# Kernel optimization log

Measured on AMD Instinct MI355X. Metric: run time of the kernel, lower is better.

The kernel has to match this reference:

```python
import jax, jax.numpy as jnp
import numpy as np
import math

HIDDEN = 256
GUMBEL_EPS = 1e-20
MASK_EPS = 1e-8
TAU = 1.0


def _gumbel(u):
    return -jnp.log(-jnp.log(u + GUMBEL_EPS) + GUMBEL_EPS)


def setup_inputs() -> dict:
    key = jax.random.key(0)
    ks = jax.random.split(key, 16)
    B, N = 16, 128
    goal_dim, obs_dim, local_dim, num_skills = 64, 128, 64, 16
    h = HIDDEN

    def lin(k, out_d, in_d):
        kw, kb = jax.random.split(k)
        bound = 1.0 / math.sqrt(in_d)
        W = jax.random.uniform(kw, (out_d, in_d), minval=-bound, maxval=bound, dtype=jnp.float32)
        b = jax.random.uniform(kb, (out_d,), minval=-bound, maxval=bound, dtype=jnp.float32)
        return W, b

    Wq, bq = lin(ks[0], h, goal_dim)
    Wk, bk = lin(ks[1], h, obs_dim)
    Wv, bv = lin(ks[2], h, obs_dim)
    Wo, bo = lin(ks[3], h, h)
    Ws, bs = lin(ks[4], num_skills, local_dim + goal_dim + h)

    return {
        "goals": jax.random.normal(ks[5], (B, N, goal_dim), dtype=jnp.float32),
        "agents": jax.random.normal(ks[6], (B, N, obs_dim), dtype=jnp.float32),
        "agents_local": jax.random.normal(ks[7], (B, N, local_dim), dtype=jnp.float32),
        "u1": jax.random.uniform(ks[8], (B, N, N), dtype=jnp.float32),
        "u2": jax.random.uniform(ks[9], (B, N, N), dtype=jnp.float32),
        "Wq": Wq, "bq": bq, "Wk": Wk, "bk": bk, "Wv": Wv, "bv": bv,
        "Wo": Wo, "bo": bo, "Ws": Ws, "bs": bs,
    }


def reference(goals, agents, agents_local, u1, u2, Wq, bq, Wk, bk, Wv, bv, Wo, bo, Ws, bs):
    # Projections
    Q = jnp.einsum('bnd,hd->bnh', goals, Wq) + bq   # [B,N,h]
    K = jnp.einsum('bmd,hd->bmh', agents, Wk) + bk  # [B,N,h]
    V = jnp.einsum('bmd,hd->bmh', agents, Wv) + bv  # [B,N,h]

    scale = math.sqrt(HIDDEN) + 1e-12
    logits = jnp.einsum('bnh,bmh->bnm', Q, K) / scale  # [B,N,N]

    # Gumbel-sigmoid mask (soft, hard=False)
    g1, g2 = _gumbel(u1), _gumbel(u2)
    mask = jax.nn.sigmoid((logits + g1 - g2) / TAU)  # [B,N,N]

    scores = logits + jnp.log(mask + MASK_EPS)
    attn = jax.nn.softmax(scores, axis=-1)  # [B,N,N]

    # info[b,n,h] = sum_m attn[b,n,m] * mask[b,n,m] * V[b,m,h]
    # (equivalent to (attn.unsqueeze(-1) * V_masked).sum(dim=2) without
    #  materializing the [B,N,N,h] V_masked tensor)
    info = jnp.einsum('bnm,bnm,bmh->bnh', attn, mask, V)

    out = jnp.einsum('bnh,gh->bng', info, Wo) + bo  # [B,N,h]

    concat = jnp.concatenate([agents_local, goals, out], axis=-1)
    logit = jnp.einsum('bnc,sc->bns', concat, Ws) + bs  # [B,N,num_skills]

    return (logit, mask, attn, out)
```

## Files before the change

kernel.cpp:

```cpp
#include <hip/hip_runtime.h>
#include <math.h>


typedef float f32x4 __attribute__((ext_vector_type(4)));
typedef short s16x8 __attribute__((ext_vector_type(8)));

#define WOBF_OFF  0
#define QBF_OFF   32768
#define KBF_OFF   294912
#define VTBF_OFF  557056

#define LOGIT_OFF 0
#define MASK_OFF  32768
#define ATTN_OFF  294912
#define OUT_OFF   557056

static __device__ __forceinline__ unsigned short f2bf(float x) {
  unsigned int u = __float_as_uint(x);
  u = (u + 0x7fffu + ((u >> 16) & 1u)) >> 16;
  return (unsigned short)u;
}
static __device__ __forceinline__ float bf2f(unsigned short h) {
  return __uint_as_float(((unsigned int)h) << 16);
}

static __device__ __forceinline__ void split8(const float* __restrict__ p,
                                              s16x8* hi, s16x8* lo) {
  float4 x0 = *(const float4*)p;
  float4 x1 = *(const float4*)(p + 4);
  float xs[8] = {x0.x, x0.y, x0.z, x0.w, x1.x, x1.y, x1.z, x1.w};
#pragma unroll
  for (int j = 0; j < 8; j++) {
    unsigned short h = f2bf(xs[j]);
    (*hi)[j] = (short)h;
    (*lo)[j] = (short)f2bf(xs[j] - bf2f(h));
  }
}

__global__ __launch_bounds__(512) void proj_k(
    const float* __restrict__ goals, const float* __restrict__ agents,
    const float* __restrict__ Wq, const float* __restrict__ bq,
    const float* __restrict__ Wk, const float* __restrict__ bk,
    const float* __restrict__ Wv, const float* __restrict__ bv,
    const float* __restrict__ Wo, float* __restrict__ ws) {
  unsigned short* qbf  = (unsigned short*)(ws + QBF_OFF);
  unsigned short* kbf  = (unsigned short*)(ws + KBF_OFF);
  unsigned short* vtbf = (unsigned short*)(ws + VTBF_OFF);
  unsigned short* wobf = (unsigned short*)(ws + WOBF_OFF);

  __shared__ __align__(16) float xg[16 * 68];
  __shared__ __align__(16) float xa[16 * 132];

  int t = threadIdx.x;
  int bid = blockIdx.x;
  int xcd = bid & 7, j = bid >> 3;
  int bb = 2 * xcd + (j & 1);
  int sub = j >> 1;
  int r0 = bb * 128 + (sub >> 1) * 16;
  int colbase = (sub & 1) * 128;

  for (int i = t; i < 1024; i += 512) xg[(i >> 6) * 68 + (i & 63)] = goals[(size_t)r0 * 64 + i];
  for (int i = t; i < 2048; i += 512) xa[(i >> 7) * 132 + (i & 127)] = agents[(size_t)r0 * 128 + i];
  if (t < 256) {
    int jj = bid * 256 + t;
    wobf[jj] = f2bf(Wo[jj]);
  }
  __syncthreads();

  int w = t >> 6, l = t & 63, lr = l & 15, lc = l >> 4;
  int oc = colbase + w * 16 + lr;

  {
    f32x4 acc = {0.f, 0.f, 0.f, 0.f};
#pragma unroll
    for (int kk = 0; kk < 2; kk++) {
      s16x8 ahi, alo, bhi, blo;
      split8(&xg[lr * 68 + kk * 32 + lc * 8], &ahi, &alo);
      split8(&Wq[(size_t)oc * 64 + kk * 32 + lc * 8], &bhi, &blo);
      acc = __builtin_amdgcn_mfma_f32_16x16x32_bf16(ahi, bhi, acc, 0, 0, 0);
      acc = __builtin_amdgcn_mfma_f32_16x16x32_bf16(alo, bhi, acc, 0, 0, 0);
      acc = __builtin_amdgcn_mfma_f32_16x16x32_bf16(ahi, blo, acc, 0, 0, 0);
    }
    float bqv = bq[oc];
#pragma unroll
    for (int q = 0; q < 4; q++)
      qbf[(size_t)(r0 + 4 * lc + q) * 256 + oc] = f2bf(acc[q] + bqv);
  }
  {
    f32x4 acc = {0.f, 0.f, 0.f, 0.f};
#pragma unroll
    for (int kk = 0; kk < 4; kk++) {
      s16x8 ahi, alo, bhi, blo;
      split8(&xa[lr * 132 + kk * 32 + lc * 8], &ahi, &alo);
      split8(&Wk[(size_t)oc * 128 + kk * 32 + lc * 8], &bhi, &blo);
      acc = __builtin_amdgcn_mfma_f32_16x16x32_bf16(ahi, bhi, acc, 0, 0, 0);
      acc = __builtin_amdgcn_mfma_f32_16x16x32_bf16(alo, bhi, acc, 0, 0, 0);
      acc = __builtin_amdgcn_mfma_f32_16x16x32_bf16(ahi, blo, acc, 0, 0, 0);
    }
    float bkv = bk[oc];
#pragma unroll
    for (int q = 0; q < 4; q++)
      kbf[(size_t)(r0 + 4 * lc + q) * 256 + oc] = f2bf(acc[q] + bkv);
  }
  {
    f32x4 acc = {0.f, 0.f, 0.f, 0.f};
#pragma unroll
    for (int kk = 0; kk < 4; kk++) {
      s16x8 ahi, alo, bhi, blo;
      split8(&xa[lr * 132 + kk * 32 + lc * 8], &ahi, &alo);
      split8(&Wv[(size_t)oc * 128 + kk * 32 + lc * 8], &bhi, &blo);
      acc = __builtin_amdgcn_mfma_f32_16x16x32_bf16(ahi, bhi, acc, 0, 0, 0);
      acc = __builtin_amdgcn_mfma_f32_16x16x32_bf16(alo, bhi, acc, 0, 0, 0);
      acc = __builtin_amdgcn_mfma_f32_16x16x32_bf16(ahi, blo, acc, 0, 0, 0);
    }
    float bvv = bv[oc];
    int m0 = r0 & 127;
#pragma unroll
    for (int q = 0; q < 4; q++)
      vtbf[(size_t)(bb * 256 + oc) * 128 + m0 + 4 * lc + q] = f2bf(acc[q] + bvv);
  }
}

__global__ __launch_bounds__(1024) void attn_k(
    const float* __restrict__ goals, const float* __restrict__ agents_local,
    const float* __restrict__ u1, const float* __restrict__ u2,
    const float* __restrict__ bo, const float* __restrict__ Wsm,
    const float* __restrict__ bs, const float* __restrict__ ws,
    float* __restrict__ out) {
  const unsigned short* Qbf  = (const unsigned short*)(ws + QBF_OFF);
  const unsigned short* Kbf  = (const unsigned short*)(ws + KBF_OFF);
  const unsigned short* VTbf = (const unsigned short*)(ws + VTBF_OFF);
  const unsigned short* Wobf = (const unsigned short*)(ws + WOBF_OFF);
  float* o_logit = out + LOGIT_OFF;
  float* o_mask  = out + MASK_OFF;
  float* o_attn  = out + ATTN_OFF;
  float* o_out   = out + OUT_OFF;

  int bid = blockIdx.x;
  int xcd = bid & 7, idx = bid >> 3;
  int b  = 2 * xcd + (idx & 1);
  int n0 = (idx >> 1) << 3;
  int rtile = n0 & 0x70;
  int soff  = n0 & 8;
  int t = threadIdx.x;
  int w = t >> 6, l = t & 63, lr = l & 15, lc = l >> 4;

  __shared__ __align__(16) float Spp[2][8][132];
  __shared__ __align__(16) unsigned short Wb[16 * 136];
  __shared__ __align__(16) unsigned short Ib[16 * 264];
  __shared__ __align__(16) float outb[8 * 260];
  __shared__ float redmax[8][2], redsum[8][2];

  int pm = t & 127, prl = t >> 7;
  int prow = b * 128 + n0 + prl;
  float uu1 = u1[(size_t)prow * 128 + pm];
  float uu2 = u2[(size_t)prow * 128 + pm];
  float bov = bo[w * 16 + lr];

  {
    int mt = w & 7, kh = w >> 3;
    const s16x8* ap = (const s16x8*)(Qbf + (size_t)(b * 128 + rtile + lr) * 256 + kh * 128);
    const s16x8* bp = (const s16x8*)(Kbf + (size_t)(b * 128 + mt * 16 + lr) * 256 + kh * 128);
    f32x4 acc = {0.f, 0.f, 0.f, 0.f};
#pragma unroll
    for (int kk = 0; kk < 4; kk++)
      acc = __builtin_amdgcn_mfma_f32_16x16x32_bf16(ap[kk * 4 + lc], bp[kk * 4 + lc], acc, 0, 0, 0);
    if ((lc >> 1) == (soff >> 3)) {
#pragma unroll
      for (int q = 0; q < 4; q++) Spp[kh][(4 * lc + q) & 7][mt * 16 + lr] = acc[q];
    }
    if (t < 544) ((unsigned int*)(Wb + (soff ^ 8) * 136))[t] = 0u;
  }
  __syncthreads();

  {
    int half = (t >> 6) & 1;
    float lg = (Spp[0][prl][pm] + Spp[1][prl][pm]) * 0.0625f;
    float g1 = -__logf(-__logf(uu1 + 1e-20f) + 1e-20f);
    float g2 = -__logf(-__logf(uu2 + 1e-20f) + 1e-20f);
    float mkv = 1.0f / (1.0f + __expf(-(lg + g1 - g2)));
    o_mask[(size_t)prow * 128 + pm] = mkv;
    float sc = lg + __logf(mkv + 1e-8f);
    float v = sc;
#pragma unroll
    for (int off = 32; off >= 1; off >>= 1) v = fmaxf(v, __shfl_xor(v, off));
    if (l == 0) redmax[prl][half] = v;
    __syncthreads();
    float rmax = fmaxf(redmax[prl][0], redmax[prl][1]);
    float e = __expf(sc - rmax);
    float s = e;
#pragma unroll
    for (int off = 32; off >= 1; off >>= 1) s += __shfl_xor(s, off);
    if (l == 0) redsum[prl][half] = s;
    __syncthreads();
    float rsum = redsum[prl][0] + redsum[prl][1];
    float attn = e / rsum;
    o_attn[(size_t)prow * 128 + pm] = attn;
    Wb[(soff + prl) * 136 + pm] = f2bf(attn * mkv);
  }
  __syncthreads();

  {
    int h0 = w * 16;
    f32x4 acc = {0.f, 0.f, 0.f, 0.f};
#pragma unroll
    for (int kk = 0; kk < 4; kk++) {
      s16x8 a = *(const s16x8*)(Wb + lr * 136 + kk * 32 + lc * 8);
      s16x8 bfr = *(const s16x8*)(VTbf + (size_t)(b * 256 + h0 + lr) * 128 + kk * 32 + lc * 8);
      acc = __builtin_amdgcn_mfma_f32_16x16x32_bf16(a, bfr, acc, 0, 0, 0);
    }
#pragma unroll
    for (int q = 0; q < 4; q++) Ib[(4 * lc + q) * 264 + h0 + lr] = f2bf(acc[q]);
  }
  __syncthreads();

  {
    int g0 = w * 16;
    f32x4 acc = {0.f, 0.f, 0.f, 0.f};
#pragma unroll
    for (int kk = 0; kk < 8; kk++) {
      s16x8 a = *(const s16x8*)(Ib + lr * 264 + kk * 32 + lc * 8);
      s16x8 bfr = *(const s16x8*)(Wobf + (size_t)(g0 + lr) * 256 + kk * 32 + lc * 8);
      acc = __builtin_amdgcn_mfma_f32_16x16x32_bf16(a, bfr, acc, 0, 0, 0);
    }
    if ((lc >> 1) == (soff >> 3)) {
#pragma unroll
      for (int q = 0; q < 4; q++) {
        int rloc = (4 * lc + q) & 7;
        float val = acc[q] + bov;
        o_out[(size_t)(b * 128 + n0 + rloc) * 256 + g0 + lr] = val;
        outb[rloc * 260 + g0 + lr] = val;
      }
    }
  }
  __syncthreads();

  {
    int rloc = t >> 7, s = (t >> 3) & 15, p = t & 7;
    int row = b * 128 + n0 + rloc;
    const float4* Ws4 = (const float4*)(Wsm + s * 384);
    const float4* lp4 = (const float4*)(agents_local + (size_t)row * 64);
    const float4* gp4 = (const float4*)(goals + (size_t)row * 64);
    float acc = 0.f;
#pragma unroll
    for (int i = 0; i < 12; i++) {
      int cc = p * 48 + i * 4;
      float4 c4;
      if (cc < 64)       c4 = lp4[cc >> 2];
      else if (cc < 128) c4 = gp4[(cc - 64) >> 2];
      else               c4 = *(const float4*)&outb[rloc * 260 + (cc - 128)];
      float4 w4 = Ws4[cc >> 2];
      acc = fmaf(w4.x, c4.x, fmaf(w4.y, c4.y, fmaf(w4.z, c4.z, fmaf(w4.w, c4.w, acc))));
    }
    acc += __shfl_xor(acc, 1);
    acc += __shfl_xor(acc, 2);
    acc += __shfl_xor(acc, 4);
    if (p == 0) o_logit[row * 16 + s] = acc + bs[s];
  }
}

extern "C" void kernel_launch(void* const* d_in, const int* in_sizes, int n_in,
                              void* d_out, int out_size, void* d_ws, size_t ws_size,
                              hipStream_t stream) {
  const float* goals        = (const float*)d_in[0];
  const float* agents       = (const float*)d_in[1];
  const float* agents_local = (const float*)d_in[2];
  const float* u1           = (const float*)d_in[3];
  const float* u2           = (const float*)d_in[4];
  const float* Wq = (const float*)d_in[5];
  const float* bq = (const float*)d_in[6];
  const float* Wk = (const float*)d_in[7];
  const float* bk = (const float*)d_in[8];
  const float* Wv = (const float*)d_in[9];
  const float* bv = (const float*)d_in[10];
  const float* Wo = (const float*)d_in[11];
  const float* bo = (const float*)d_in[12];
  const float* Wsm = (const float*)d_in[13];
  const float* bs  = (const float*)d_in[14];
  float* out = (float*)d_out;
  float* ws  = (float*)d_ws;

  proj_k<<<256, 512, 0, stream>>>(goals, agents, Wq, bq, Wk, bk, Wv, bv, Wo, ws);
  attn_k<<<256, 1024, 0, stream>>>(goals, agents_local, u1, u2, bo, Wsm, bs, ws, out);
}
```

Measured before the change: 33.88 us.

## Fold Wo into V projection via precomputed Wo·Wv and drop attention output GEMM

Adds a small kernel that precomputes Wo·Wv and Wo·bv as split hi/lo bf16 weights. The value projection then produces V·Wo^T directly, so the attention kernel does a single attn·VWo matmul and drops the intermediate info buffer, one sync and the second GEMM. Prefetches the VWo fragments early, and uses nontemporal loads/stores for the gumbel inputs and outputs. The cost is an extra kernel launch and double-width hi/lo V storage.

```diff
diff --git a/kernel.cpp b/kernel.cpp
--- a/kernel.cpp
+++ b/kernel.cpp
@@ -5,10 +5,13 @@
 typedef float f32x4 __attribute__((ext_vector_type(4)));
 typedef short s16x8 __attribute__((ext_vector_type(8)));
 
-#define WOBF_OFF  0
-#define QBF_OFF   32768
-#define KBF_OFF   294912
-#define VTBF_OFF  557056
+#define WVO_HI    0
+#define WVO_LO    16384
+#define BVO       32768
+#define QBF_OFF   33024
+#define KBF_OFF   295168
+#define VWOTH_OFF 557312
+#define VWOTL_OFF 819456
 
 #define LOGIT_OFF 0
 #define MASK_OFF  32768
@@ -23,7 +26,6 @@
 static __device__ __forceinline__ float bf2f(unsigned short h) {
   return __uint_as_float(((unsigned int)h) << 16);
 }
-
 static __device__ __forceinline__ void split8(const float* __restrict__ p,
                                               s16x8* hi, s16x8* lo) {
   float4 x0 = *(const float4*)p;
@@ -36,17 +38,80 @@
     (*lo)[j] = (short)f2bf(xs[j] - bf2f(h));
   }
 }
+#define MFMA(a, b, c) __builtin_amdgcn_mfma_f32_16x16x32_bf16((a), (b), (c), 0, 0, 0)
+
+__global__ __launch_bounds__(256) void wvo_k(
+    const float* __restrict__ Wo, const float* __restrict__ Wv,
+    const float* __restrict__ bv, float* __restrict__ ws) {
+  unsigned short* wvoh = (unsigned short*)(ws + WVO_HI);
+  unsigned short* wvol = (unsigned short*)(ws + WVO_LO);
+  float* bvo = ws + BVO;
+
+  __shared__ float wv_l[256 * 64];
+
+  int t = threadIdx.x, bid = blockIdx.x;
+  int gt = bid >> 1, dh = bid & 1;
+  int g0t = gt * 16;
+
+  for (int i = t; i < 16384; i += 256) {
+    int h = i >> 6, dl = i & 63;
+    wv_l[h * 64 + dl] = Wv[h * 128 + dh * 64 + dl];
+  }
+  if (dh == 0) {
+    int gl = t >> 4, p = t & 15;
+    const float* wor = Wo + (size_t)(g0t + gl) * 256 + p * 16;
+    float bacc = 0.f;
+#pragma unroll
+    for (int j = 0; j < 16; j++) bacc = fmaf(bv[p * 16 + j], wor[j], bacc);
+    bacc += __shfl_xor(bacc, 1);
+    bacc += __shfl_xor(bacc, 2);
+    bacc += __shfl_xor(bacc, 4);
+    bacc += __shfl_xor(bacc, 8);
+    if (p == 0) bvo[g0t + gl] = bacc;
+  }
+  __syncthreads();
+
+  int w = t >> 6, l = t & 63, lr = l & 15, lc = l >> 4;
+  int d0 = dh * 64 + w * 16, dl0 = w * 16;
+  f32x4 acc = {0.f, 0.f, 0.f, 0.f};
+#pragma unroll
+  for (int kk = 0; kk < 8; kk++) {
+    s16x8 ah, al;
+    split8(&Wo[(size_t)(g0t + lr) * 256 + kk * 32 + lc * 8], &ah, &al);
+    s16x8 bh, bl;
+#pragma unroll
+    for (int j = 0; j < 8; j++) {
+      float x = wv_l[(kk * 32 + lc * 8 + j) * 64 + dl0 + lr];
+      unsigned short h2 = f2bf(x);
+      bh[j] = (short)h2;
+      bl[j] = (short)f2bf(x - bf2f(h2));
+    }
+    acc = MFMA(ah, bh, acc);
+    acc = MFMA(al, bh, acc);
+    acc = MFMA(ah, bl, acc);
+  }
+#pragma unroll
+  for (int q = 0; q < 4; q++) {
+    int g = g0t + 4 * lc + q;
+    float x = acc[q];
+    unsigned short hi = f2bf(x);
+    wvoh[g * 128 + d0 + lr] = hi;
+    wvol[g * 128 + d0 + lr] = f2bf(x - bf2f(hi));
+  }
+}
 
 __global__ __launch_bounds__(512) void proj_k(
     const float* __restrict__ goals, const float* __restrict__ agents,
     const float* __restrict__ Wq, const float* __restrict__ bq,
     const float* __restrict__ Wk, const float* __restrict__ bk,
-    const float* __restrict__ Wv, const float* __restrict__ bv,
-    const float* __restrict__ Wo, float* __restrict__ ws) {
-  unsigned short* qbf  = (unsigned short*)(ws + QBF_OFF);
-  unsigned short* kbf  = (unsigned short*)(ws + KBF_OFF);
-  unsigned short* vtbf = (unsigned short*)(ws + VTBF_OFF);
-  unsigned short* wobf = (unsigned short*)(ws + WOBF_OFF);
+    float* __restrict__ ws) {
+  unsigned short* qbf   = (unsigned short*)(ws + QBF_OFF);
+  unsigned short* kbf   = (unsigned short*)(ws + KBF_OFF);
+  unsigned short* vwoth = (unsigned short*)(ws + VWOTH_OFF);
+  unsigned short* vwotl = (unsigned short*)(ws + VWOTL_OFF);
+  const unsigned short* wvoh = (const unsigned short*)(ws + WVO_HI);
+  const unsigned short* wvol = (const unsigned short*)(ws + WVO_LO);
+  const float* bvo = ws + BVO;
 
   __shared__ __align__(16) float xg[16 * 68];
   __shared__ __align__(16) float xa[16 * 132];
@@ -54,17 +119,13 @@
   int t = threadIdx.x;
   int bid = blockIdx.x;
   int xcd = bid & 7, j = bid >> 3;
-  int bb = 2 * xcd + (j & 1);
+  int batch = 2 * xcd + (j & 1);
   int sub = j >> 1;
-  int r0 = bb * 128 + (sub >> 1) * 16;
+  int r0 = batch * 128 + (sub >> 1) * 16;
   int colbase = (sub & 1) * 128;
 
   for (int i = t; i < 1024; i += 512) xg[(i >> 6) * 68 + (i & 63)] = goals[(size_t)r0 * 64 + i];
   for (int i = t; i < 2048; i += 512) xa[(i >> 7) * 132 + (i & 127)] = agents[(size_t)r0 * 128 + i];
-  if (t < 256) {
-    int jj = bid * 256 + t;
-    wobf[jj] = f2bf(Wo[jj]);
-  }
   __syncthreads();
 
   int w = t >> 6, l = t & 63, lr = l & 15, lc = l >> 4;
@@ -77,9 +138,9 @@
       s16x8 ahi, alo, bhi, blo;
       split8(&xg[lr * 68 + kk * 32 + lc * 8], &ahi, &alo);
       split8(&Wq[(size_t)oc * 64 + kk * 32 + lc * 8], &bhi, &blo);
-      acc = __builtin_amdgcn_mfma_f32_16x16x32_bf16(ahi, bhi, acc, 0, 0, 0);
-      acc = __builtin_amdgcn_mfma_f32_16x16x32_bf16(alo, bhi, acc, 0, 0, 0);
-      acc = __builtin_amdgcn_mfma_f32_16x16x32_bf16(ahi, blo, acc, 0, 0, 0);
+      acc = MFMA(ahi, bhi, acc);
+      acc = MFMA(alo, bhi, acc);
+      acc = MFMA(ahi, blo, acc);
     }
     float bqv = bq[oc];
 #pragma unroll
@@ -93,9 +154,9 @@
       s16x8 ahi, alo, bhi, blo;
       split8(&xa[lr * 132 + kk * 32 + lc * 8], &ahi, &alo);
       split8(&Wk[(size_t)oc * 128 + kk * 32 + lc * 8], &bhi, &blo);
-      acc = __builtin_amdgcn_mfma_f32_16x16x32_bf16(ahi, bhi, acc, 0, 0, 0);
-      acc = __builtin_amdgcn_mfma_f32_16x16x32_bf16(alo, bhi, acc, 0, 0, 0);
-      acc = __builtin_amdgcn_mfma_f32_16x16x32_bf16(ahi, blo, acc, 0, 0, 0);
+      acc = MFMA(ahi, bhi, acc);
+      acc = MFMA(alo, bhi, acc);
+      acc = MFMA(ahi, blo, acc);
     }
     float bkv = bk[oc];
 #pragma unroll
@@ -106,18 +167,24 @@
     f32x4 acc = {0.f, 0.f, 0.f, 0.f};
 #pragma unroll
     for (int kk = 0; kk < 4; kk++) {
-      s16x8 ahi, alo, bhi, blo;
+      s16x8 ahi, alo;
       split8(&xa[lr * 132 + kk * 32 + lc * 8], &ahi, &alo);
-      split8(&Wv[(size_t)oc * 128 + kk * 32 + lc * 8], &bhi, &blo);
-      acc = __builtin_amdgcn_mfma_f32_16x16x32_bf16(ahi, bhi, acc, 0, 0, 0);
-      acc = __builtin_amdgcn_mfma_f32_16x16x32_bf16(alo, bhi, acc, 0, 0, 0);
-      acc = __builtin_amdgcn_mfma_f32_16x16x32_bf16(ahi, blo, acc, 0, 0, 0);
-    }
-    float bvv = bv[oc];
+      s16x8 bh = *(const s16x8*)(wvoh + (size_t)oc * 128 + kk * 32 + lc * 8);
+      s16x8 bl = *(const s16x8*)(wvol + (size_t)oc * 128 + kk * 32 + lc * 8);
+      acc = MFMA(ahi, bh, acc);
+      acc = MFMA(alo, bh, acc);
+      acc = MFMA(ahi, bl, acc);
+    }
+    float bvov = bvo[oc];
     int m0 = r0 & 127;
 #pragma unroll
-    for (int q = 0; q < 4; q++)
-      vtbf[(size_t)(bb * 256 + oc) * 128 + m0 + 4 * lc + q] = f2bf(acc[q] + bvv);
+    for (int q = 0; q < 4; q++) {
+      float x = acc[q] + bvov;
+      unsigned short hi = f2bf(x);
+      size_t idx = (size_t)(batch * 256 + oc) * 128 + m0 + 4 * lc + q;
+      vwoth[idx] = hi;
+      vwotl[idx] = f2bf(x - bf2f(hi));
+    }
   }
 }
 
@@ -127,10 +194,10 @@
     const float* __restrict__ bo, const float* __restrict__ Wsm,
     const float* __restrict__ bs, const float* __restrict__ ws,
     float* __restrict__ out) {
-  const unsigned short* Qbf  = (const unsigned short*)(ws + QBF_OFF);
-  const unsigned short* Kbf  = (const unsigned short*)(ws + KBF_OFF);
-  const unsigned short* VTbf = (const unsigned short*)(ws + VTBF_OFF);
-  const unsigned short* Wobf = (const unsigned short*)(ws + WOBF_OFF);
+  const unsigned short* Qbf   = (const unsigned short*)(ws + QBF_OFF);
+  const unsigned short* Kbf   = (const unsigned short*)(ws + KBF_OFF);
+  const unsigned short* VWOTH = (const unsigned short*)(ws + VWOTH_OFF);
+  const unsigned short* VWOTL = (const unsigned short*)(ws + VWOTL_OFF);
   float* o_logit = out + LOGIT_OFF;
   float* o_mask  = out + MASK_OFF;
   float* o_attn  = out + ATTN_OFF;
@@ -147,15 +214,19 @@
 
   __shared__ __align__(16) float Spp[2][8][132];
   __shared__ __align__(16) unsigned short Wb[16 * 136];
-  __shared__ __align__(16) unsigned short Ib[16 * 264];
   __shared__ __align__(16) float outb[8 * 260];
   __shared__ float redmax[8][2], redsum[8][2];
 
   int pm = t & 127, prl = t >> 7;
   int prow = b * 128 + n0 + prl;
-  float uu1 = u1[(size_t)prow * 128 + pm];
-  float uu2 = u2[(size_t)prow * 128 + pm];
-  float bov = bo[w * 16 + lr];
+  float uu1 = __builtin_nontemporal_load(&u1[(size_t)prow * 128 + pm]);
+  float uu2 = __builtin_nontemporal_load(&u2[(size_t)prow * 128 + pm]);
+  int g0 = w * 16;
+  float bov = bo[g0 + lr];
+  const s16x8* vhp = (const s16x8*)(VWOTH + (size_t)(b * 256 + g0 + lr) * 128);
+  const s16x8* vlp = (const s16x8*)(VWOTL + (size_t)(b * 256 + g0 + lr) * 128);
+  s16x8 fh0 = vhp[lc],      fh1 = vhp[4 + lc],  fh2 = vhp[8 + lc],  fh3 = vhp[12 + lc];
+  s16x8 fl0 = vlp[lc],      fl1 = vlp[4 + lc],  fl2 = vlp[8 + lc],  fl3 = vlp[12 + lc];
 
   {
     int mt = w & 7, kh = w >> 3;
@@ -164,7 +235,7 @@
     f32x4 acc = {0.f, 0.f, 0.f, 0.f};
 #pragma unroll
     for (int kk = 0; kk < 4; kk++)
-      acc = __builtin_amdgcn_mfma_f32_16x16x32_bf16(ap[kk * 4 + lc], bp[kk * 4 + lc], acc, 0, 0, 0);
+      acc = MFMA(ap[kk * 4 + lc], bp[kk * 4 + lc], acc);
     if ((lc >> 1) == (soff >> 3)) {
 #pragma unroll
       for (int q = 0; q < 4; q++) Spp[kh][(4 * lc + q) & 7][mt * 16 + lr] = acc[q];
@@ -179,7 +250,7 @@
     float g1 = -__logf(-__logf(uu1 + 1e-20f) + 1e-20f);
     float g2 = -__logf(-__logf(uu2 + 1e-20f) + 1e-20f);
     float mkv = 1.0f / (1.0f + __expf(-(lg + g1 - g2)));
-    o_mask[(size_t)prow * 128 + pm] = mkv;
+    __builtin_nontemporal_store(mkv, &o_mask[(size_t)prow * 128 + pm]);
     float sc = lg + __logf(mkv + 1e-8f);
     float v = sc;
 #pragma unroll
@@ -195,40 +266,31 @@
     __syncthreads();
     float rsum = redsum[prl][0] + redsum[prl][1];
     float attn = e / rsum;
-    o_attn[(size_t)prow * 128 + pm] = attn;
+    __builtin_nontemporal_store(attn, &o_attn[(size_t)prow * 128 + pm]);
     Wb[(soff + prl) * 136 + pm] = f2bf(attn * mkv);
   }
   __syncthreads();
 
   {
-    int h0 = w * 16;
-    f32x4 acc = {0.f, 0.f, 0.f, 0.f};
-#pragma unroll
-    for (int kk = 0; kk < 4; kk++) {
-      s16x8 a = *(const s16x8*)(Wb + lr * 136 + kk * 32 + lc * 8);
-      s16x8 bfr = *(const s16x8*)(VTbf + (size_t)(b * 256 + h0 + lr) * 128 + kk * 32 + lc * 8);
-      acc = __builtin_amdgcn_mfma_f32_16x16x32_bf16(a, bfr, acc, 0, 0, 0);
-    }
-#pragma unroll
-    for (int q = 0; q < 4; q++) Ib[(4 * lc + q) * 264 + h0 + lr] = f2bf(acc[q]);
-  }
-  __syncthreads();
-
-  {
-    int g0 = w * 16;
-    f32x4 acc = {0.f, 0.f, 0.f, 0.f};
-#pragma unroll
-    for (int kk = 0; kk < 8; kk++) {
-      s16x8 a = *(const s16x8*)(Ib + lr * 264 + kk * 32 + lc * 8);
-      s16x8 bfr = *(const s16x8*)(Wobf + (size_t)(g0 + lr) * 256 + kk * 32 + lc * 8);
-      acc = __builtin_amdgcn_mfma_f32_16x16x32_bf16(a, bfr, acc, 0, 0, 0);
-    }
+    s16x8 a0 = *(const s16x8*)(Wb + lr * 136 + 0 * 32 + lc * 8);
+    s16x8 a1 = *(const s16x8*)(Wb + lr * 136 + 1 * 32 + lc * 8);
+    s16x8 a2 = *(const s16x8*)(Wb + lr * 136 + 2 * 32 + lc * 8);
+    s16x8 a3 = *(const s16x8*)(Wb + lr * 136 + 3 * 32 + lc * 8);
+    f32x4 acc = {0.f, 0.f, 0.f, 0.f};
+    acc = MFMA(a0, fh0, acc);
+    acc = MFMA(a1, fh1, acc);
+    acc = MFMA(a2, fh2, acc);
+    acc = MFMA(a3, fh3, acc);
+    acc = MFMA(a0, fl0, acc);
+    acc = MFMA(a1, fl1, acc);
+    acc = MFMA(a2, fl2, acc);
+    acc = MFMA(a3, fl3, acc);
     if ((lc >> 1) == (soff >> 3)) {
 #pragma unroll
       for (int q = 0; q < 4; q++) {
         int rloc = (4 * lc + q) & 7;
         float val = acc[q] + bov;
-        o_out[(size_t)(b * 128 + n0 + rloc) * 256 + g0 + lr] = val;
+        __builtin_nontemporal_store(val, &o_out[(size_t)(b * 128 + n0 + rloc) * 256 + g0 + lr]);
         outb[rloc * 260 + g0 + lr] = val;
       }
     }
@@ -255,7 +317,7 @@
     acc += __shfl_xor(acc, 1);
     acc += __shfl_xor(acc, 2);
     acc += __shfl_xor(acc, 4);
-    if (p == 0) o_logit[row * 16 + s] = acc + bs[s];
+    if (p == 0) __builtin_nontemporal_store(acc + bs[s], &o_logit[row * 16 + s]);
   }
 }
 
@@ -280,6 +342,7 @@
   float* out = (float*)d_out;
   float* ws  = (float*)d_ws;
 
-  proj_k<<<256, 512, 0, stream>>>(goals, agents, Wq, bq, Wk, bk, Wv, bv, Wo, ws);
+  wvo_k<<<32, 256, 0, stream>>>(Wo, Wv, bv, ws);
+  proj_k<<<256, 512, 0, stream>>>(goals, agents, Wq, bq, Wk, bk, ws);
   attn_k<<<256, 1024, 0, stream>>>(goals, agents_local, u1, u2, bo, Wsm, bs, ws, out);
 }
```

Measured after the change: 38.18 us. +12.7%, slower.

## Precompute V·Wo^T in projection kernel and drop second GEMM from attention

Applied to the files above, without the earlier changes.

Uses associativity to fold the output projection into V: the projection kernel now computes VWo = V·Wo^T per batch (via an LDS-staged bf16 V tile and an extra MFMA pass), so the attention kernel does one attn·mask × VWo GEMM instead of two chained GEMMs with an LDS round-trip and extra barrier. The projection grid changes to 128 blocks of 1024 threads covering all 256 output columns. VWo fragments are prefetched early in attn_k, and streaming inputs and outputs use nontemporal loads and stores. This changes the rounding path, since V·Wo is now rounded to bf16 before the attention weights are applied.

```diff
diff --git a/kernel.cpp b/kernel.cpp
--- a/kernel.cpp
+++ b/kernel.cpp
@@ -5,10 +5,9 @@
 typedef float f32x4 __attribute__((ext_vector_type(4)));
 typedef short s16x8 __attribute__((ext_vector_type(8)));
 
-#define WOBF_OFF  0
-#define QBF_OFF   32768
-#define KBF_OFF   294912
-#define VTBF_OFF  557056
+#define QBF_OFF   0
+#define KBF_OFF   262144
+#define VWOT_OFF  524288
 
 #define LOGIT_OFF 0
 #define MASK_OFF  32768
@@ -23,7 +22,6 @@
 static __device__ __forceinline__ float bf2f(unsigned short h) {
   return __uint_as_float(((unsigned int)h) << 16);
 }
-
 static __device__ __forceinline__ void split8(const float* __restrict__ p,
                                               s16x8* hi, s16x8* lo) {
   float4 x0 = *(const float4*)p;
@@ -36,8 +34,22 @@
     (*lo)[j] = (short)f2bf(xs[j] - bf2f(h));
   }
 }
-
-__global__ __launch_bounds__(512) void proj_k(
+static __device__ __forceinline__ unsigned int cvtpk(float a, float b) {
+  unsigned int d;
+  asm("v_cvt_pk_bf16_f32 %0, %1, %2" : "=v"(d) : "v"(a), "v"(b));
+  return d;
+}
+static __device__ __forceinline__ s16x8 g2f8(const float* __restrict__ p) {
+  float4 x = *(const float4*)p;
+  float4 y = *(const float4*)(p + 4);
+  union { unsigned int u[4]; s16x8 v; } r;
+  r.u[0] = cvtpk(x.x, x.y); r.u[1] = cvtpk(x.z, x.w);
+  r.u[2] = cvtpk(y.x, y.y); r.u[3] = cvtpk(y.z, y.w);
+  return r.v;
+}
+#define MFMA(a, b, c) __builtin_amdgcn_mfma_f32_16x16x32_bf16((a), (b), (c), 0, 0, 0)
+
+__global__ __launch_bounds__(1024) void projv_k(
     const float* __restrict__ goals, const float* __restrict__ agents,
     const float* __restrict__ Wq, const float* __restrict__ bq,
     const float* __restrict__ Wk, const float* __restrict__ bk,
@@ -45,30 +57,31 @@
     const float* __restrict__ Wo, float* __restrict__ ws) {
   unsigned short* qbf  = (unsigned short*)(ws + QBF_OFF);
   unsigned short* kbf  = (unsigned short*)(ws + KBF_OFF);
-  unsigned short* vtbf = (unsigned short*)(ws + VTBF_OFF);
-  unsigned short* wobf = (unsigned short*)(ws + WOBF_OFF);
+  unsigned short* vwot = (unsigned short*)(ws + VWOT_OFF);
 
   __shared__ __align__(16) float xg[16 * 68];
   __shared__ __align__(16) float xa[16 * 132];
+  __shared__ __align__(16) unsigned short vbuf[16 * 264];
 
   int t = threadIdx.x;
   int bid = blockIdx.x;
   int xcd = bid & 7, j = bid >> 3;
-  int bb = 2 * xcd + (j & 1);
-  int sub = j >> 1;
-  int r0 = bb * 128 + (sub >> 1) * 16;
-  int colbase = (sub & 1) * 128;
-
-  for (int i = t; i < 1024; i += 512) xg[(i >> 6) * 68 + (i & 63)] = goals[(size_t)r0 * 64 + i];
-  for (int i = t; i < 2048; i += 512) xa[(i >> 7) * 132 + (i & 127)] = agents[(size_t)r0 * 128 + i];
-  if (t < 256) {
-    int jj = bid * 256 + t;
-    wobf[jj] = f2bf(Wo[jj]);
+  int batch = 2 * xcd + (j & 1);
+  int rw = j >> 1;
+  int r0 = batch * 128 + rw * 16;
+  int m0 = rw * 16;
+
+  xg[(t >> 6) * 68 + (t & 63)] = goals[(size_t)r0 * 64 + (t & 1023)];
+  {
+    int i = t;
+    xa[(i >> 7) * 132 + (i & 127)] = agents[(size_t)r0 * 128 + i];
+    i = t + 1024;
+    xa[(i >> 7) * 132 + (i & 127)] = agents[(size_t)r0 * 128 + i];
   }
   __syncthreads();
 
   int w = t >> 6, l = t & 63, lr = l & 15, lc = l >> 4;
-  int oc = colbase + w * 16 + lr;
+  int oc = w * 16 + lr;
 
   {
     f32x4 acc = {0.f, 0.f, 0.f, 0.f};
@@ -77,9 +90,9 @@
       s16x8 ahi, alo, bhi, blo;
       split8(&xg[lr * 68 + kk * 32 + lc * 8], &ahi, &alo);
       split8(&Wq[(size_t)oc * 64 + kk * 32 + lc * 8], &bhi, &blo);
-      acc = __builtin_amdgcn_mfma_f32_16x16x32_bf16(ahi, bhi, acc, 0, 0, 0);
-      acc = __builtin_amdgcn_mfma_f32_16x16x32_bf16(alo, bhi, acc, 0, 0, 0);
-      acc = __builtin_amdgcn_mfma_f32_16x16x32_bf16(ahi, blo, acc, 0, 0, 0);
+      acc = MFMA(ahi, bhi, acc);
+      acc = MFMA(alo, bhi, acc);
+      acc = MFMA(ahi, blo, acc);
     }
     float bqv = bq[oc];
 #pragma unroll
@@ -93,9 +106,9 @@
       s16x8 ahi, alo, bhi, blo;
       split8(&xa[lr * 132 + kk * 32 + lc * 8], &ahi, &alo);
       split8(&Wk[(size_t)oc * 128 + kk * 32 + lc * 8], &bhi, &blo);
-      acc = __builtin_amdgcn_mfma_f32_16x16x32_bf16(ahi, bhi, acc, 0, 0, 0);
-      acc = __builtin_amdgcn_mfma_f32_16x16x32_bf16(alo, bhi, acc, 0, 0, 0);
-      acc = __builtin_amdgcn_mfma_f32_16x16x32_bf16(ahi, blo, acc, 0, 0, 0);
+      acc = MFMA(ahi, bhi, acc);
+      acc = MFMA(alo, bhi, acc);
+      acc = MFMA(ahi, blo, acc);
     }
     float bkv = bk[oc];
 #pragma unroll
@@ -109,15 +122,27 @@
       s16x8 ahi, alo, bhi, blo;
       split8(&xa[lr * 132 + kk * 32 + lc * 8], &ahi, &alo);
       split8(&Wv[(size_t)oc * 128 + kk * 32 + lc * 8], &bhi, &blo);
-      acc = __builtin_amdgcn_mfma_f32_16x16x32_bf16(ahi, bhi, acc, 0, 0, 0);
-      acc = __builtin_amdgcn_mfma_f32_16x16x32_bf16(alo, bhi, acc, 0, 0, 0);
-      acc = __builtin_amdgcn_mfma_f32_16x16x32_bf16(ahi, blo, acc, 0, 0, 0);
+      acc = MFMA(ahi, bhi, acc);
+      acc = MFMA(alo, bhi, acc);
+      acc = MFMA(ahi, blo, acc);
     }
     float bvv = bv[oc];
-    int m0 = r0 & 127;
-#pragma unroll
-    for (int q = 0; q < 4; q++)
-      vtbf[(size_t)(bb * 256 + oc) * 128 + m0 + 4 * lc + q] = f2bf(acc[q] + bvv);
+#pragma unroll
+    for (int q = 0; q < 4; q++)
+      vbuf[(4 * lc + q) * 264 + oc] = f2bf(acc[q] + bvv);
+  }
+  __syncthreads();
+
+  {
+    f32x4 acc = {0.f, 0.f, 0.f, 0.f};
+#pragma unroll
+    for (int kk = 0; kk < 8; kk++) {
+      s16x8 a = *(const s16x8*)(vbuf + lr * 264 + kk * 32 + lc * 8);
+      acc = MFMA(a, g2f8(&Wo[(size_t)oc * 256 + kk * 32 + lc * 8]), acc);
+    }
+#pragma unroll
+    for (int q = 0; q < 4; q++)
+      vwot[(size_t)(batch * 256 + oc) * 128 + m0 + 4 * lc + q] = f2bf(acc[q]);
   }
 }
 
@@ -129,8 +154,7 @@
     float* __restrict__ out) {
   const unsigned short* Qbf  = (const unsigned short*)(ws + QBF_OFF);
   const unsigned short* Kbf  = (const unsigned short*)(ws + KBF_OFF);
-  const unsigned short* VTbf = (const unsigned short*)(ws + VTBF_OFF);
-  const unsigned short* Wobf = (const unsigned short*)(ws + WOBF_OFF);
+  const unsigned short* VWOT = (const unsigned short*)(ws + VWOT_OFF);
   float* o_logit = out + LOGIT_OFF;
   float* o_mask  = out + MASK_OFF;
   float* o_attn  = out + ATTN_OFF;
@@ -147,15 +171,17 @@
 
   __shared__ __align__(16) float Spp[2][8][132];
   __shared__ __align__(16) unsigned short Wb[16 * 136];
-  __shared__ __align__(16) unsigned short Ib[16 * 264];
   __shared__ __align__(16) float outb[8 * 260];
   __shared__ float redmax[8][2], redsum[8][2];
 
   int pm = t & 127, prl = t >> 7;
   int prow = b * 128 + n0 + prl;
-  float uu1 = u1[(size_t)prow * 128 + pm];
-  float uu2 = u2[(size_t)prow * 128 + pm];
-  float bov = bo[w * 16 + lr];
+  float uu1 = __builtin_nontemporal_load(&u1[(size_t)prow * 128 + pm]);
+  float uu2 = __builtin_nontemporal_load(&u2[(size_t)prow * 128 + pm]);
+  int g0 = w * 16;
+  float bov = bo[g0 + lr];
+  const s16x8* vhp = (const s16x8*)(VWOT + (size_t)(b * 256 + g0 + lr) * 128);
+  s16x8 fh0 = vhp[lc], fh1 = vhp[4 + lc], fh2 = vhp[8 + lc], fh3 = vhp[12 + lc];
 
   {
     int mt = w & 7, kh = w >> 3;
@@ -164,7 +190,7 @@
     f32x4 acc = {0.f, 0.f, 0.f, 0.f};
 #pragma unroll
     for (int kk = 0; kk < 4; kk++)
-      acc = __builtin_amdgcn_mfma_f32_16x16x32_bf16(ap[kk * 4 + lc], bp[kk * 4 + lc], acc, 0, 0, 0);
+      acc = MFMA(ap[kk * 4 + lc], bp[kk * 4 + lc], acc);
     if ((lc >> 1) == (soff >> 3)) {
 #pragma unroll
       for (int q = 0; q < 4; q++) Spp[kh][(4 * lc + q) & 7][mt * 16 + lr] = acc[q];
@@ -179,7 +205,7 @@
     float g1 = -__logf(-__logf(uu1 + 1e-20f) + 1e-20f);
     float g2 = -__logf(-__logf(uu2 + 1e-20f) + 1e-20f);
     float mkv = 1.0f / (1.0f + __expf(-(lg + g1 - g2)));
-    o_mask[(size_t)prow * 128 + pm] = mkv;
+    __builtin_nontemporal_store(mkv, &o_mask[(size_t)prow * 128 + pm]);
     float sc = lg + __logf(mkv + 1e-8f);
     float v = sc;
 #pragma unroll
@@ -195,40 +221,27 @@
     __syncthreads();
     float rsum = redsum[prl][0] + redsum[prl][1];
     float attn = e / rsum;
-    o_attn[(size_t)prow * 128 + pm] = attn;
+    __builtin_nontemporal_store(attn, &o_attn[(size_t)prow * 128 + pm]);
     Wb[(soff + prl) * 136 + pm] = f2bf(attn * mkv);
   }
   __syncthreads();
 
   {
-    int h0 = w * 16;
-    f32x4 acc = {0.f, 0.f, 0.f, 0.f};
-#pragma unroll
-    for (int kk = 0; kk < 4; kk++) {
-      s16x8 a = *(const s16x8*)(Wb + lr * 136 + kk * 32 + lc * 8);
-      s16x8 bfr = *(const s16x8*)(VTbf + (size_t)(b * 256 + h0 + lr) * 128 + kk * 32 + lc * 8);
-      acc = __builtin_amdgcn_mfma_f32_16x16x32_bf16(a, bfr, acc, 0, 0, 0);
-    }
-#pragma unroll
-    for (int q = 0; q < 4; q++) Ib[(4 * lc + q) * 264 + h0 + lr] = f2bf(acc[q]);
-  }
-  __syncthreads();
-
-  {
-    int g0 = w * 16;
-    f32x4 acc = {0.f, 0.f, 0.f, 0.f};
-#pragma unroll
-    for (int kk = 0; kk < 8; kk++) {
-      s16x8 a = *(const s16x8*)(Ib + lr * 264 + kk * 32 + lc * 8);
-      s16x8 bfr = *(const s16x8*)(Wobf + (size_t)(g0 + lr) * 256 + kk * 32 + lc * 8);
-      acc = __builtin_amdgcn_mfma_f32_16x16x32_bf16(a, bfr, acc, 0, 0, 0);
-    }
+    s16x8 a0 = *(const s16x8*)(Wb + lr * 136 + 0 * 32 + lc * 8);
+    s16x8 a1 = *(const s16x8*)(Wb + lr * 136 + 1 * 32 + lc * 8);
+    s16x8 a2 = *(const s16x8*)(Wb + lr * 136 + 2 * 32 + lc * 8);
+    s16x8 a3 = *(const s16x8*)(Wb + lr * 136 + 3 * 32 + lc * 8);
+    f32x4 acc = {0.f, 0.f, 0.f, 0.f};
+    acc = MFMA(a0, fh0, acc);
+    acc = MFMA(a1, fh1, acc);
+    acc = MFMA(a2, fh2, acc);
+    acc = MFMA(a3, fh3, acc);
     if ((lc >> 1) == (soff >> 3)) {
 #pragma unroll
       for (int q = 0; q < 4; q++) {
         int rloc = (4 * lc + q) & 7;
         float val = acc[q] + bov;
-        o_out[(size_t)(b * 128 + n0 + rloc) * 256 + g0 + lr] = val;
+        __builtin_nontemporal_store(val, &o_out[(size_t)(b * 128 + n0 + rloc) * 256 + g0 + lr]);
         outb[rloc * 260 + g0 + lr] = val;
       }
     }
@@ -255,7 +268,7 @@
     acc += __shfl_xor(acc, 1);
     acc += __shfl_xor(acc, 2);
     acc += __shfl_xor(acc, 4);
-    if (p == 0) o_logit[row * 16 + s] = acc + bs[s];
+    if (p == 0) __builtin_nontemporal_store(acc + bs[s], &o_logit[row * 16 + s]);
   }
 }
 
@@ -280,6 +293,6 @@
   float* out = (float*)d_out;
   float* ws  = (float*)d_ws;
 
-  proj_k<<<256, 512, 0, stream>>>(goals, agents, Wq, bq, Wk, bk, Wv, bv, Wo, ws);
+  projv_k<<<128, 1024, 0, stream>>>(goals, agents, Wq, bq, Wk, bk, Wv, bv, Wo, ws);
   attn_k<<<256, 1024, 0, stream>>>(goals, agents_local, u1, u2, bo, Wsm, bs, ws, out);
 }
```

Result: slower. 40.86 us (+20.6%).
